# Performance work log

Hardware: AMD Instinct MI355X
Metric: run time of the kernel (lower is better)

The kernel has to match this reference:

```python
import jax, jax.numpy as jnp
import numpy as np
import math

B, S, D, H = 2, 2048, 1024, 16
DK = D // H


def setup_inputs() -> dict:
    key = jax.random.key(0)
    ks = jax.random.split(key, 11)
    f = jnp.float32
    return {
        "query": jax.random.normal(ks[0], (B, S, D), f),
        "key": jax.random.normal(ks[1], (B, S, D), f),
        "value": jax.random.normal(ks[2], (B, S, D), f),
        "wq": jax.random.normal(ks[3], (D, D), f) * 0.02,
        "bq": jnp.zeros((D,), f),
        "wk": jax.random.normal(ks[4], (D, D), f) * 0.02,
        "bk": jnp.zeros((D,), f),
        "wv": jax.random.normal(ks[5], (D, D), f) * 0.02,
        "bv": jnp.zeros((D,), f),
        "wo": jax.random.normal(ks[6], (D, D), f) * 0.02,
        "bo": jnp.zeros((D,), f),
    }


def reference(query, key, value, wq, bq, wk, bk, wv, bv, wo, bo):
    # Linear projections (torch Linear: y = x @ W.T + b)
    q = query @ wq.T + bq
    k = key @ wk.T + bk
    v = value @ wv.T + bv
    # [B,S,D] -> [B,H,S,DK]
    q = q.reshape(B, S, H, DK).transpose(0, 2, 1, 3)
    k = k.reshape(B, S, H, DK).transpose(0, 2, 1, 3)
    v = v.reshape(B, S, H, DK).transpose(0, 2, 1, 3)
    scores = jnp.einsum("bhqd,bhkd->bhqk", q, k) / math.sqrt(DK)
    causal = jnp.triu(jnp.ones((S, S), dtype=bool), k=1)  # strict upper triangle masked
    scores = jnp.where(causal, -jnp.inf, scores)
    attn = jax.nn.softmax(scores, axis=-1)  # dropout is identity in eval (p=0)
    x = jnp.einsum("bhqk,bhkd->bhqd", attn, v)
    x = x.transpose(0, 2, 1, 3).reshape(B, S, D)
    return x @ wo.T + bo
```

## Files before the change

### kernel.cpp

```cpp
#include <hip/hip_runtime.h>
#include <math.h>

#define BB 2
#define SS 2048
#define DD 1024
#define HH 16
#define DKK 64
#define MM (BB * SS)
#define KK DD
#define VSTR 2176

typedef __attribute__((ext_vector_type(8))) short short8;
typedef __attribute__((ext_vector_type(4))) float floatx4;

__device__ inline unsigned short f2bf(float x) {
    unsigned int u = __float_as_uint(x);
    u += 0x7fffu + ((u >> 16) & 1u);
    return (unsigned short)(u >> 16);
}

__device__ inline unsigned int pkbf(float a, float b) {
    return (__float_as_uint(b) & 0xffff0000u) | (__float_as_uint(a) >> 16);
}

__device__ inline void cast4f(const float* __restrict__ in, unsigned short* __restrict__ out, int i) {
    const float4 v = *(const float4*)(in + i);
    unsigned long long pk = (unsigned long long)f2bf(v.x)
                          | ((unsigned long long)f2bf(v.y) << 16)
                          | ((unsigned long long)f2bf(v.z) << 32)
                          | ((unsigned long long)f2bf(v.w) << 48);
    *(unsigned long long*)(out + i) = pk;
}

__global__ __launch_bounds__(256) void cast_all(const float* __restrict__ q, const float* __restrict__ k,
                                                const float* __restrict__ v,
                                                const float* __restrict__ wq, const float* __restrict__ wk,
                                                const float* __restrict__ wv, const float* __restrict__ wo,
                                                unsigned short* __restrict__ oq, unsigned short* __restrict__ ok,
                                                unsigned short* __restrict__ ov,
                                                unsigned short* __restrict__ owq, unsigned short* __restrict__ owk,
                                                unsigned short* __restrict__ owv, unsigned short* __restrict__ owo) {
    const int tid = blockIdx.x * 256 + threadIdx.x;
    #pragma unroll
    for (int it = 0; it < 8; ++it) {
        const int g = tid + it * 524288;
        const float* in;
        unsigned short* out;
        int idx;
        if (g < 3145728) {
            const int w = g >> 20;
            idx = g & 1048575;
            in  = (w == 0) ? q : (w == 1) ? k : v;
            out = (w == 0) ? oq : (w == 1) ? ok : ov;
        } else {
            const int gw = g - 3145728;
            const int w = gw >> 18;
            idx = gw & 262143;
            in  = (w == 0) ? wq : (w == 1) ? wk : (w == 2) ? wv : wo;
            out = (w == 0) ? owq : (w == 1) ? owk : (w == 2) ? owv : owo;
        }
        cast4f(in, out, idx * 4);
    }
}

#define GLDS(gp, lp) __builtin_amdgcn_global_load_lds( \
    (const __attribute__((address_space(1))) void*)(gp), \
    (__attribute__((address_space(3))) void*)(lp), 16, 0, 0)

#define SCHED0() __builtin_amdgcn_sched_barrier(0)
#define BAR()    __builtin_amdgcn_s_barrier()
#define WAITL0() asm volatile("s_waitcnt lgkmcnt(0)" ::: "memory")
#define WAITV(n) asm volatile("s_waitcnt vmcnt(" #n ")" ::: "memory")

__device__ __forceinline__ void gemm128_body(const unsigned short* __restrict__ A,
                                             const unsigned short* __restrict__ W,
                                             int m0, int n0,
                                             unsigned short* __restrict__ As,
                                             unsigned short* __restrict__ Bs,
                                             floatx4 (&acc)[4][4]) {
    const int t    = threadIdx.x;
    const int lane = t & 63;
    const int wave = t >> 6;
    const int col  = lane & 15;
    const int quad = lane >> 4;
    const int wm   = (wave >> 1) * 64;
    const int wn   = (wave & 1) * 64;

    const int r  = t >> 3;
    const int cs = t & 7;

    const int sA0 = (quad ^ (col & 7)) * 8;
    const int sA1 = ((quad + 4) ^ (col & 7)) * 8;

    auto stage = [&](int kt, int pb) {
        const int k0 = kt * 64;
        #pragma unroll
        for (int g = 0; g < 4; ++g) {
            const int row = g * 32 + r;
            const int ksw = (cs ^ (row & 7)) * 8;
            GLDS(A + (size_t)(m0 + row) * KK + k0 + ksw,
                 &As[pb * (128 * 64) + row * 64 + cs * 8]);
        }
        #pragma unroll
        for (int g = 0; g < 4; ++g) {
            const int row = g * 32 + r;
            const int ksw = (cs ^ (row & 7)) * 8;
            GLDS(W + (size_t)(n0 + row) * KK + k0 + ksw,
                 &Bs[pb * (128 * 64) + row * 64 + cs * 8]);
        }
    };

    stage(0, 0);
    WAITV(0); SCHED0(); BAR(); SCHED0();

    const int NK = KK / 64;
    for (int kt = 0; kt < NK; ++kt) {
        const int p = kt & 1;
        if (kt + 1 < NK) stage(kt + 1, p ^ 1);

        const unsigned short* Ab = &As[p * (128 * 64)];
        const unsigned short* Bb = &Bs[p * (128 * 64)];
        short8 a0[4], a1[4], b0[4], b1[4];
        #pragma unroll
        for (int i = 0; i < 4; ++i) {
            const unsigned short* ar = Ab + (wm + i * 16 + col) * 64;
            a0[i] = *(const short8*)(ar + sA0);
            a1[i] = *(const short8*)(ar + sA1);
        }
        #pragma unroll
        for (int j = 0; j < 4; ++j) {
            const unsigned short* br = Bb + (wn + j * 16 + col) * 64;
            b0[j] = *(const short8*)(br + sA0);
            b1[j] = *(const short8*)(br + sA1);
        }

        __builtin_amdgcn_s_setprio(1);
        #pragma unroll
        for (int i = 0; i < 4; ++i)
            #pragma unroll
            for (int j = 0; j < 4; ++j)
                acc[i][j] = __builtin_amdgcn_mfma_f32_16x16x32_bf16(a0[i], b0[j], acc[i][j], 0, 0, 0);
        #pragma unroll
        for (int i = 0; i < 4; ++i)
            #pragma unroll
            for (int j = 0; j < 4; ++j)
                acc[i][j] = __builtin_amdgcn_mfma_f32_16x16x32_bf16(a1[i], b1[j], acc[i][j], 0, 0, 0);
        __builtin_amdgcn_s_setprio(0);

        WAITL0(); SCHED0();
        if (kt + 1 < NK) { WAITV(0); }
        SCHED0(); BAR(); SCHED0();
    }
}

__global__ __launch_bounds__(256, 2) void gemm_qkv(const unsigned short* __restrict__ qB,
                                                   const unsigned short* __restrict__ kB,
                                                   const unsigned short* __restrict__ vB,
                                                   const unsigned short* __restrict__ wqB,
                                                   const unsigned short* __restrict__ wkB,
                                                   const unsigned short* __restrict__ wvB,
                                                   const float* __restrict__ bq,
                                                   const float* __restrict__ bk,
                                                   const float* __restrict__ bv,
                                                   unsigned short* __restrict__ Qh,
                                                   unsigned short* __restrict__ Kh,
                                                   unsigned short* __restrict__ Vt) {
    __shared__ __align__(16) unsigned short As[2 * 128 * 64];
    __shared__ __align__(16) unsigned short Bs[2 * 128 * 64];

    const int bid   = blockIdx.x;
    const int wgid  = (bid & 7) * 96 + (bid >> 3);
    const int which = wgid >> 8;
    const int tile  = wgid & 255;
    const int m0    = (tile >> 3) * 128;
    const int n0    = (tile & 7) * 128;

    const unsigned short* A = (which == 0) ? qB : (which == 1) ? kB : vB;
    const unsigned short* W = (which == 0) ? wqB : (which == 1) ? wkB : wvB;
    const float* bias       = (which == 0) ? bq : (which == 1) ? bk : bv;

    floatx4 acc[4][4] = {};
    gemm128_body(A, W, m0, n0, As, Bs, acc);

    const int t    = threadIdx.x;
    const int lane = t & 63;
    const int wave = t >> 6;
    const int col  = lane & 15;
    const int quad = lane >> 4;
    const int wm   = (wave >> 1) * 64;
    const int wn   = (wave & 1) * 64;

    #pragma unroll
    for (int i = 0; i < 4; ++i) {
        #pragma unroll
        for (int j = 0; j < 4; ++j) {
            const int n  = n0 + wn + j * 16 + col;
            const float bv0 = bias[n];
            const int h = n >> 6, dk = n & 63;
            const int mb  = m0 + wm + i * 16 + quad * 4;
            const int bdx = mb >> 11, s = mb & 2047;
            if (which != 2) {
                unsigned short* O = (which == 0) ? Qh : Kh;
                #pragma unroll
                for (int rr = 0; rr < 4; ++rr)
                    O[(((size_t)(bdx * HH + h)) * SS + (s + rr)) * DKK + dk] = f2bf(acc[i][j][rr] + bv0);
            } else {
                unsigned short* vp = Vt + (((size_t)(bdx * HH + h)) * DKK + dk) * VSTR + s;
                uint2 w;
                w.x = (unsigned int)f2bf(acc[i][j][0] + bv0) | ((unsigned int)f2bf(acc[i][j][1] + bv0) << 16);
                w.y = (unsigned int)f2bf(acc[i][j][2] + bv0) | ((unsigned int)f2bf(acc[i][j][3] + bv0) << 16);
                *(uint2*)vp = w;
            }
        }
    }
}

__global__ __launch_bounds__(256, 2) void gemm_out(const unsigned short* __restrict__ A,
                                                   const unsigned short* __restrict__ W,
                                                   const float* __restrict__ bias,
                                                   float* __restrict__ C) {
    __shared__ __align__(16) unsigned short As[2 * 128 * 64];
    __shared__ __align__(16) unsigned short Bs[2 * 128 * 64];

    const int bid  = blockIdx.x;
    const int wgid = (bid & 7) * 32 + (bid >> 3);
    const int m0   = (wgid >> 3) * 128;
    const int n0   = (wgid & 7) * 128;

    floatx4 acc[4][4] = {};
    gemm128_body(A, W, m0, n0, As, Bs, acc);

    const int t    = threadIdx.x;
    const int lane = t & 63;
    const int wave = t >> 6;
    const int col  = lane & 15;
    const int quad = lane >> 4;
    const int wm   = (wave >> 1) * 64;
    const int wn   = (wave & 1) * 64;

    #pragma unroll
    for (int i = 0; i < 4; ++i) {
        #pragma unroll
        for (int j = 0; j < 4; ++j) {
            const int n = n0 + wn + j * 16 + col;
            const float bv0 = bias[n];
            #pragma unroll
            for (int rr = 0; rr < 4; ++rr) {
                const int m = m0 + wm + i * 16 + quad * 4 + rr;
                C[(size_t)m * DD + n] = acc[i][j][rr] + bv0;
            }
        }
    }
}

#define C1 0.18033688011112042f
#define C2 11.541560327111707f
#define MFMA __builtin_amdgcn_mfma_f32_16x16x32_bf16

__global__ __launch_bounds__(512) void attn_mfma(const unsigned short* __restrict__ Qh,
                                                 const unsigned short* __restrict__ Kh,
                                                 const unsigned short* __restrict__ Vt,
                                                 unsigned short* __restrict__ X) {
    __shared__ __align__(16) unsigned short Ks[2][64 * 64];
    __shared__ __align__(16) unsigned short Vs[2][64 * 64];
    __shared__ __align__(16) unsigned short Plds[8][16 * 40];

    const int t    = threadIdx.x;
    const int lane = t & 63;
    const int wave = t >> 6;
    const int col  = lane & 15;
    const int quad = lane >> 4;

    const int lin = blockIdx.x;
    const int bh  = (lin & 7) + 8 * ((lin >> 3) & 3);
    const int pr  = lin >> 5;
    const int b   = bh / HH, h = bh % HH;

    const int cX  = (wave < 4) ? (31 - pr) : pr;
    const int q0  = cX * 64 + (wave & 3) * 16;
    const int nst = 32 - pr;

    const unsigned short* Kb = Kh + (size_t)bh * SS * DKK;
    const unsigned short* Vb = Vt + (size_t)bh * DKK * VSTR;

    const int r0  = t >> 3;
    const int sg0 = ((t & 7) ^ (r0 & 7)) * 8;

    unsigned short* Pw = &Plds[wave][0];

    const unsigned short* Qb = Qh + ((size_t)bh * SS + q0) * DKK;
    const short8 qa0 = *(const short8*)(Qb + (size_t)col * DKK + quad * 8);
    const short8 qa1 = *(const short8*)(Qb + (size_t)col * DKK + 32 + quad * 8);

    floatx4 o0 = {0.f, 0.f, 0.f, 0.f}, o1 = o0, o2 = o0, o3 = o0;
    float lp = 0.f;

    const int ksA = ((quad)      ^ (col & 7)) * 8;
    const int ksB = ((quad | 4)  ^ (col & 7)) * 8;

    GLDS(Kb + (size_t)r0 * DKK + sg0,  &Ks[0][t * 8]);
    GLDS(Vb + (size_t)r0 * VSTR + sg0, &Vs[0][t * 8]);

    int cur = 0;
    for (int kb = 0; kb < nst; ++kb) {
        __syncthreads();

        if (kb + 1 < nst) {
            const int jn = (kb + 1) * 64;
            const int nx = cur ^ 1;
            GLDS(Kb + (size_t)(jn + r0) * DKK + sg0,  &Ks[nx][t * 8]);
            GLDS(Vb + (size_t)r0 * VSTR + jn + sg0,   &Vs[nx][t * 8]);
        }

        const unsigned short* Kp = &Ks[cur][0];
        const unsigned short* Vp = &Vs[cur][0];

        #pragma unroll
        for (int hh = 0; hh < 2; ++hh) {
            const int j0 = kb * 64 + hh * 32;
            if (j0 < q0 + 16) {
                const short8 k0 = *(const short8*)(Kp + (hh * 32 + col) * 64 + ksA);
                const short8 k1 = *(const short8*)(Kp + (hh * 32 + col) * 64 + ksB);
                const short8 k2 = *(const short8*)(Kp + (hh * 32 + col + 16) * 64 + ksA);
                const short8 k3 = *(const short8*)(Kp + (hh * 32 + col + 16) * 64 + ksB);

                floatx4 t0 = {0.f, 0.f, 0.f, 0.f}, t1 = t0;
                __builtin_amdgcn_s_setprio(1);
                t0 = MFMA(k0, qa0, t0, 0, 0, 0);
                t0 = MFMA(k1, qa1, t0, 0, 0, 0);
                t1 = MFMA(k2, qa0, t1, 0, 0, 0);
                t1 = MFMA(k3, qa1, t1, 0, 0, 0);
                __builtin_amdgcn_s_setprio(0);

                float p[8];
                if (j0 + 31 > q0) {
                    const int lim = q0 + col - j0;
                    #pragma unroll
                    for (int r = 0; r < 4; ++r) {
                        p[r]     = (quad * 4 + r      <= lim) ? __builtin_exp2f(fmaf(t0[r], C1, -C2)) : 0.f;
                        p[4 + r] = (16 + quad * 4 + r <= lim) ? __builtin_exp2f(fmaf(t1[r], C1, -C2)) : 0.f;
                    }
                } else {
                    #pragma unroll
                    for (int r = 0; r < 4; ++r) {
                        p[r]     = __builtin_exp2f(fmaf(t0[r], C1, -C2));
                        p[4 + r] = __builtin_exp2f(fmaf(t1[r], C1, -C2));
                    }
                }
                lp += (p[0] + p[1]) + (p[2] + p[3]) + (p[4] + p[5]) + (p[6] + p[7]);

                uint2 w0 = { pkbf(p[0], p[1]), pkbf(p[2], p[3]) };
                uint2 w1 = { pkbf(p[4], p[5]), pkbf(p[6], p[7]) };
                *(uint2*)(Pw + col * 40 + quad * 4)      = w0;
                *(uint2*)(Pw + col * 40 + 16 + quad * 4) = w1;

                const short8 pb = *(const short8*)(Pw + col * 40 + quad * 8);
                const int vs = hh ? ksB : ksA;
                const short8 v0 = *(const short8*)(Vp + (col)      * 64 + vs);
                const short8 v1 = *(const short8*)(Vp + (col + 16) * 64 + vs);
                const short8 v2 = *(const short8*)(Vp + (col + 32) * 64 + vs);
                const short8 v3 = *(const short8*)(Vp + (col + 48) * 64 + vs);
                __builtin_amdgcn_s_setprio(1);
                o0 = MFMA(v0, pb, o0, 0, 0, 0);
                o1 = MFMA(v1, pb, o1, 0, 0, 0);
                o2 = MFMA(v2, pb, o2, 0, 0, 0);
                o3 = MFMA(v3, pb, o3, 0, 0, 0);
                __builtin_amdgcn_s_setprio(0);
            }
        }

        cur ^= 1;
    }

    lp += __shfl_xor(lp, 16, 64);
    lp += __shfl_xor(lp, 32, 64);
    const float li = 1.f / lp;

    unsigned short* Xp = X + ((size_t)(b * SS + q0 + col)) * DD + h * DKK + quad * 4;
    {
        uint2 w;
        w.x = (unsigned int)f2bf(o0[0] * li) | ((unsigned int)f2bf(o0[1] * li) << 16);
        w.y = (unsigned int)f2bf(o0[2] * li) | ((unsigned int)f2bf(o0[3] * li) << 16);
        *(uint2*)(Xp + 0) = w;
        w.x = (unsigned int)f2bf(o1[0] * li) | ((unsigned int)f2bf(o1[1] * li) << 16);
        w.y = (unsigned int)f2bf(o1[2] * li) | ((unsigned int)f2bf(o1[3] * li) << 16);
        *(uint2*)(Xp + 16) = w;
        w.x = (unsigned int)f2bf(o2[0] * li) | ((unsigned int)f2bf(o2[1] * li) << 16);
        w.y = (unsigned int)f2bf(o2[2] * li) | ((unsigned int)f2bf(o2[3] * li) << 16);
        *(uint2*)(Xp + 32) = w;
        w.x = (unsigned int)f2bf(o3[0] * li) | ((unsigned int)f2bf(o3[1] * li) << 16);
        w.y = (unsigned int)f2bf(o3[2] * li) | ((unsigned int)f2bf(o3[3] * li) << 16);
        *(uint2*)(Xp + 48) = w;
    }
}

extern "C" void kernel_launch(void* const* d_in, const int* in_sizes, int n_in,
                              void* d_out, int out_size, void* d_ws, size_t ws_size,
                              hipStream_t stream) {
    const float* query = (const float*)d_in[0];
    const float* key   = (const float*)d_in[1];
    const float* value = (const float*)d_in[2];
    const float* wq    = (const float*)d_in[3];
    const float* bq    = (const float*)d_in[4];
    const float* wk    = (const float*)d_in[5];
    const float* bk    = (const float*)d_in[6];
    const float* wv    = (const float*)d_in[7];
    const float* bv    = (const float*)d_in[8];
    const float* wo    = (const float*)d_in[9];
    const float* bo    = (const float*)d_in[10];

    char* ws = (char*)d_ws;
    const size_t MB = 1024 * 1024;
    unsigned short* qB  = (unsigned short*)(ws);
    unsigned short* kB  = (unsigned short*)(ws + 8 * MB);
    unsigned short* vB  = (unsigned short*)(ws + 16 * MB);
    unsigned short* wqB = (unsigned short*)(ws + 24 * MB);
    unsigned short* wkB = (unsigned short*)(ws + 26 * MB);
    unsigned short* wvB = (unsigned short*)(ws + 28 * MB);
    unsigned short* woB = (unsigned short*)(ws + 30 * MB);
    unsigned short* Qh  = (unsigned short*)(ws + 32 * MB);
    unsigned short* Kh  = (unsigned short*)(ws + 40 * MB);
    unsigned short* Vt  = (unsigned short*)(ws + 48 * MB);
    unsigned short* Xb  = qB;

    cast_all<<<2048, 256, 0, stream>>>(query, key, value, wq, wk, wv, wo,
                                       qB, kB, vB, wqB, wkB, wvB, woB);

    gemm_qkv<<<768, 256, 0, stream>>>(qB, kB, vB, wqB, wkB, wvB, bq, bk, bv, Qh, Kh, Vt);

    attn_mfma<<<512, 512, 0, stream>>>(Qh, Kh, Vt, Xb);

    gemm_out<<<256, 256, 0, stream>>>(Xb, woB, bo, (float*)d_out);
}
```

Measured before the change: 219.8 us.

## Restructure cast grid, vectorize Q/K epilogue via swapped MFMA, narrow out-GEMM tiles

The cast kernel now launches one block per 1024-element chunk instead of looping eight times per thread. The QKV GEMM swaps the MFMA operands for the Q/K path, so each lane holds four consecutive head dims and can write them as one packed 8-byte store instead of scalar 2-byte scatters. The output GEMM moves to 128x64 tiles with 512 blocks, which gives more waves on the device for a GEMM that only had 256 tiles. The cost is more launched blocks and lower per-block reuse of the A tile in the output GEMM.

```diff
diff --git a/kernel.cpp b/kernel.cpp
--- a/kernel.cpp
+++ b/kernel.cpp
@@ -23,6 +23,10 @@
     return (__float_as_uint(b) & 0xffff0000u) | (__float_as_uint(a) >> 16);
 }
 
+__device__ inline unsigned int pkbf_rne(float a, float b) {
+    return (unsigned int)f2bf(a) | ((unsigned int)f2bf(b) << 16);
+}
+
 __device__ inline void cast4f(const float* __restrict__ in, unsigned short* __restrict__ out, int i) {
     const float4 v = *(const float4*)(in + i);
     unsigned long long pk = (unsigned long long)f2bf(v.x)
@@ -40,27 +44,22 @@
                                                 unsigned short* __restrict__ ov,
                                                 unsigned short* __restrict__ owq, unsigned short* __restrict__ owk,
                                                 unsigned short* __restrict__ owv, unsigned short* __restrict__ owo) {
-    const int tid = blockIdx.x * 256 + threadIdx.x;
-    #pragma unroll
-    for (int it = 0; it < 8; ++it) {
-        const int g = tid + it * 524288;
-        const float* in;
-        unsigned short* out;
-        int idx;
-        if (g < 3145728) {
-            const int w = g >> 20;
-            idx = g & 1048575;
-            in  = (w == 0) ? q : (w == 1) ? k : v;
-            out = (w == 0) ? oq : (w == 1) ? ok : ov;
-        } else {
-            const int gw = g - 3145728;
-            const int w = gw >> 18;
-            idx = gw & 262143;
-            in  = (w == 0) ? wq : (w == 1) ? wk : (w == 2) ? wv : wo;
-            out = (w == 0) ? owq : (w == 1) ? owk : (w == 2) ? owv : owo;
-        }
-        cast4f(in, out, idx * 4);
-    }
+    const int blk = blockIdx.x;
+    const float* in;
+    unsigned short* out;
+    int idx;
+    if (blk < 12288) {
+        const int w = blk >> 12;
+        idx = blk & 4095;
+        in  = (w == 0) ? q : (w == 1) ? k : v;
+        out = (w == 0) ? oq : (w == 1) ? ok : ov;
+    } else {
+        const int w = (blk - 12288) >> 10;
+        idx = (blk - 12288) & 1023;
+        in  = (w == 0) ? wq : (w == 1) ? wk : (w == 2) ? wv : wo;
+        out = (w == 0) ? owq : (w == 1) ? owk : (w == 2) ? owv : owo;
+    }
+    cast4f(in, out, (idx * 256 + threadIdx.x) * 4);
 }
 
 #define GLDS(gp, lp) __builtin_amdgcn_global_load_lds( \
@@ -72,19 +71,21 @@
 #define WAITL0() asm volatile("s_waitcnt lgkmcnt(0)" ::: "memory")
 #define WAITV(n) asm volatile("s_waitcnt vmcnt(" #n ")" ::: "memory")
 
-__device__ __forceinline__ void gemm128_body(const unsigned short* __restrict__ A,
-                                             const unsigned short* __restrict__ W,
-                                             int m0, int n0,
-                                             unsigned short* __restrict__ As,
-                                             unsigned short* __restrict__ Bs,
-                                             floatx4 (&acc)[4][4]) {
+template<int BN, int SWAP>
+__device__ __forceinline__ void gemm_body2(const unsigned short* __restrict__ A,
+                                           const unsigned short* __restrict__ W,
+                                           int m0, int n0,
+                                           unsigned short* __restrict__ As,
+                                           unsigned short* __restrict__ Bs,
+                                           floatx4 (&acc)[4][BN / 32]) {
+    constexpr int NJ = BN / 32;
     const int t    = threadIdx.x;
     const int lane = t & 63;
     const int wave = t >> 6;
     const int col  = lane & 15;
     const int quad = lane >> 4;
     const int wm   = (wave >> 1) * 64;
-    const int wn   = (wave & 1) * 64;
+    const int wn   = (wave & 1) * (BN / 2);
 
     const int r  = t >> 3;
     const int cs = t & 7;
@@ -102,11 +103,11 @@
                  &As[pb * (128 * 64) + row * 64 + cs * 8]);
         }
         #pragma unroll
-        for (int g = 0; g < 4; ++g) {
+        for (int g = 0; g < BN / 32; ++g) {
             const int row = g * 32 + r;
             const int ksw = (cs ^ (row & 7)) * 8;
             GLDS(W + (size_t)(n0 + row) * KK + k0 + ksw,
-                 &Bs[pb * (128 * 64) + row * 64 + cs * 8]);
+                 &Bs[pb * (BN * 64) + row * 64 + cs * 8]);
         }
     };
 
@@ -119,8 +120,8 @@
         if (kt + 1 < NK) stage(kt + 1, p ^ 1);
 
         const unsigned short* Ab = &As[p * (128 * 64)];
-        const unsigned short* Bb = &Bs[p * (128 * 64)];
-        short8 a0[4], a1[4], b0[4], b1[4];
+        const unsigned short* Bb = &Bs[p * (BN * 64)];
+        short8 a0[4], a1[4], b0[NJ], b1[NJ];
         #pragma unroll
         for (int i = 0; i < 4; ++i) {
             const unsigned short* ar = Ab + (wm + i * 16 + col) * 64;
@@ -128,7 +129,7 @@
             a1[i] = *(const short8*)(ar + sA1);
         }
         #pragma unroll
-        for (int j = 0; j < 4; ++j) {
+        for (int j = 0; j < NJ; ++j) {
             const unsigned short* br = Bb + (wn + j * 16 + col) * 64;
             b0[j] = *(const short8*)(br + sA0);
             b1[j] = *(const short8*)(br + sA1);
@@ -138,13 +139,21 @@
         #pragma unroll
         for (int i = 0; i < 4; ++i)
             #pragma unroll
-            for (int j = 0; j < 4; ++j)
-                acc[i][j] = __builtin_amdgcn_mfma_f32_16x16x32_bf16(a0[i], b0[j], acc[i][j], 0, 0, 0);
+            for (int j = 0; j < NJ; ++j) {
+                if constexpr (SWAP)
+                    acc[i][j] = __builtin_amdgcn_mfma_f32_16x16x32_bf16(b0[j], a0[i], acc[i][j], 0, 0, 0);
+                else
+                    acc[i][j] = __builtin_amdgcn_mfma_f32_16x16x32_bf16(a0[i], b0[j], acc[i][j], 0, 0, 0);
+            }
         #pragma unroll
         for (int i = 0; i < 4; ++i)
             #pragma unroll
-            for (int j = 0; j < 4; ++j)
-                acc[i][j] = __builtin_amdgcn_mfma_f32_16x16x32_bf16(a1[i], b1[j], acc[i][j], 0, 0, 0);
+            for (int j = 0; j < NJ; ++j) {
+                if constexpr (SWAP)
+                    acc[i][j] = __builtin_amdgcn_mfma_f32_16x16x32_bf16(b1[j], a1[i], acc[i][j], 0, 0, 0);
+                else
+                    acc[i][j] = __builtin_amdgcn_mfma_f32_16x16x32_bf16(a1[i], b1[j], acc[i][j], 0, 0, 0);
+            }
         __builtin_amdgcn_s_setprio(0);
 
         WAITL0(); SCHED0();
@@ -179,9 +188,6 @@
     const unsigned short* W = (which == 0) ? wqB : (which == 1) ? wkB : wvB;
     const float* bias       = (which == 0) ? bq : (which == 1) ? bk : bv;
 
-    floatx4 acc[4][4] = {};
-    gemm128_body(A, W, m0, n0, As, Bs, acc);
-
     const int t    = threadIdx.x;
     const int lane = t & 63;
     const int wave = t >> 6;
@@ -190,25 +196,41 @@
     const int wm   = (wave >> 1) * 64;
     const int wn   = (wave & 1) * 64;
 
-    #pragma unroll
-    for (int i = 0; i < 4; ++i) {
-        #pragma unroll
-        for (int j = 0; j < 4; ++j) {
-            const int n  = n0 + wn + j * 16 + col;
-            const float bv0 = bias[n];
-            const int h = n >> 6, dk = n & 63;
-            const int mb  = m0 + wm + i * 16 + quad * 4;
+    floatx4 acc[4][4] = {};
+
+    if (which != 2) {
+        gemm_body2<128, 1>(A, W, m0, n0, As, Bs, acc);
+        unsigned short* O = (which == 0) ? Qh : Kh;
+        #pragma unroll
+        for (int i = 0; i < 4; ++i) {
+            const int mb  = m0 + wm + i * 16 + col;
             const int bdx = mb >> 11, s = mb & 2047;
-            if (which != 2) {
-                unsigned short* O = (which == 0) ? Qh : Kh;
-                #pragma unroll
-                for (int rr = 0; rr < 4; ++rr)
-                    O[(((size_t)(bdx * HH + h)) * SS + (s + rr)) * DKK + dk] = f2bf(acc[i][j][rr] + bv0);
-            } else {
+            #pragma unroll
+            for (int j = 0; j < 4; ++j) {
+                const int n  = n0 + wn + j * 16 + quad * 4;
+                const float4 b4 = *(const float4*)(bias + n);
+                const int h = n >> 6, dk = n & 63;
+                uint2 w;
+                w.x = pkbf_rne(acc[i][j][0] + b4.x, acc[i][j][1] + b4.y);
+                w.y = pkbf_rne(acc[i][j][2] + b4.z, acc[i][j][3] + b4.w);
+                *(uint2*)(O + (((size_t)(bdx * HH + h)) * SS + s) * DKK + dk) = w;
+            }
+        }
+    } else {
+        gemm_body2<128, 0>(A, W, m0, n0, As, Bs, acc);
+        #pragma unroll
+        for (int i = 0; i < 4; ++i) {
+            #pragma unroll
+            for (int j = 0; j < 4; ++j) {
+                const int n  = n0 + wn + j * 16 + col;
+                const float bv0 = bias[n];
+                const int h = n >> 6, dk = n & 63;
+                const int mb  = m0 + wm + i * 16 + quad * 4;
+                const int bdx = mb >> 11, s = mb & 2047;
                 unsigned short* vp = Vt + (((size_t)(bdx * HH + h)) * DKK + dk) * VSTR + s;
                 uint2 w;
-                w.x = (unsigned int)f2bf(acc[i][j][0] + bv0) | ((unsigned int)f2bf(acc[i][j][1] + bv0) << 16);
-                w.y = (unsigned int)f2bf(acc[i][j][2] + bv0) | ((unsigned int)f2bf(acc[i][j][3] + bv0) << 16);
+                w.x = pkbf_rne(acc[i][j][0] + bv0, acc[i][j][1] + bv0);
+                w.y = pkbf_rne(acc[i][j][2] + bv0, acc[i][j][3] + bv0);
                 *(uint2*)vp = w;
             }
         }
@@ -220,15 +242,15 @@
                                                    const float* __restrict__ bias,
                                                    float* __restrict__ C) {
     __shared__ __align__(16) unsigned short As[2 * 128 * 64];
-    __shared__ __align__(16) unsigned short Bs[2 * 128 * 64];
+    __shared__ __align__(16) unsigned short Bs[2 * 64 * 64];
 
     const int bid  = blockIdx.x;
-    const int wgid = (bid & 7) * 32 + (bid >> 3);
-    const int m0   = (wgid >> 3) * 128;
-    const int n0   = (wgid & 7) * 128;
-
-    floatx4 acc[4][4] = {};
-    gemm128_body(A, W, m0, n0, As, Bs, acc);
+    const int wgid = (bid & 7) * 64 + (bid >> 3);
+    const int m0   = (wgid >> 4) * 128;
+    const int n0   = (wgid & 15) * 64;
+
+    floatx4 acc[4][2] = {};
+    gemm_body2<64, 0>(A, W, m0, n0, As, Bs, acc);
 
     const int t    = threadIdx.x;
     const int lane = t & 63;
@@ -236,12 +258,12 @@
     const int col  = lane & 15;
     const int quad = lane >> 4;
     const int wm   = (wave >> 1) * 64;
-    const int wn   = (wave & 1) * 64;
+    const int wn   = (wave & 1) * 32;
 
     #pragma unroll
     for (int i = 0; i < 4; ++i) {
         #pragma unroll
-        for (int j = 0; j < 4; ++j) {
+        for (int j = 0; j < 2; ++j) {
             const int n = n0 + wn + j * 16 + col;
             const float bv0 = bias[n];
             #pragma unroll
@@ -336,15 +358,15 @@
                 if (j0 + 31 > q0) {
                     const int lim = q0 + col - j0;
                     #pragma unroll
-                    for (int r = 0; r < 4; ++r) {
-                        p[r]     = (quad * 4 + r      <= lim) ? __builtin_exp2f(fmaf(t0[r], C1, -C2)) : 0.f;
-                        p[4 + r] = (16 + quad * 4 + r <= lim) ? __builtin_exp2f(fmaf(t1[r], C1, -C2)) : 0.f;
+                    for (int rr = 0; rr < 4; ++rr) {
+                        p[rr]     = (quad * 4 + rr      <= lim) ? __builtin_exp2f(fmaf(t0[rr], C1, -C2)) : 0.f;
+                        p[4 + rr] = (16 + quad * 4 + rr <= lim) ? __builtin_exp2f(fmaf(t1[rr], C1, -C2)) : 0.f;
                     }
                 } else {
                     #pragma unroll
-                    for (int r = 0; r < 4; ++r) {
-                        p[r]     = __builtin_exp2f(fmaf(t0[r], C1, -C2));
-                        p[4 + r] = __builtin_exp2f(fmaf(t1[r], C1, -C2));
+                    for (int rr = 0; rr < 4; ++rr) {
+                        p[rr]     = __builtin_exp2f(fmaf(t0[rr], C1, -C2));
+                        p[4 + rr] = __builtin_exp2f(fmaf(t1[rr], C1, -C2));
                     }
                 }
                 lp += (p[0] + p[1]) + (p[2] + p[3]) + (p[4] + p[5]) + (p[6] + p[7]);
@@ -379,17 +401,17 @@
     unsigned short* Xp = X + ((size_t)(b * SS + q0 + col)) * DD + h * DKK + quad * 4;
     {
         uint2 w;
-        w.x = (unsigned int)f2bf(o0[0] * li) | ((unsigned int)f2bf(o0[1] * li) << 16);
-        w.y = (unsigned int)f2bf(o0[2] * li) | ((unsigned int)f2bf(o0[3] * li) << 16);
+        w.x = pkbf_rne(o0[0] * li, o0[1] * li);
+        w.y = pkbf_rne(o0[2] * li, o0[3] * li);
         *(uint2*)(Xp + 0) = w;
-        w.x = (unsigned int)f2bf(o1[0] * li) | ((unsigned int)f2bf(o1[1] * li) << 16);
-        w.y = (unsigned int)f2bf(o1[2] * li) | ((unsigned int)f2bf(o1[3] * li) << 16);
+        w.x = pkbf_rne(o1[0] * li, o1[1] * li);
+        w.y = pkbf_rne(o1[2] * li, o1[3] * li);
         *(uint2*)(Xp + 16) = w;
-        w.x = (unsigned int)f2bf(o2[0] * li) | ((unsigned int)f2bf(o2[1] * li) << 16);
-        w.y = (unsigned int)f2bf(o2[2] * li) | ((unsigned int)f2bf(o2[3] * li) << 16);
+        w.x = pkbf_rne(o2[0] * li, o2[1] * li);
+        w.y = pkbf_rne(o2[2] * li, o2[3] * li);
         *(uint2*)(Xp + 32) = w;
-        w.x = (unsigned int)f2bf(o3[0] * li) | ((unsigned int)f2bf(o3[1] * li) << 16);
-        w.y = (unsigned int)f2bf(o3[2] * li) | ((unsigned int)f2bf(o3[3] * li) << 16);
+        w.x = pkbf_rne(o3[0] * li, o3[1] * li);
+        w.y = pkbf_rne(o3[2] * li, o3[3] * li);
         *(uint2*)(Xp + 48) = w;
     }
 }
@@ -423,12 +445,12 @@
     unsigned short* Vt  = (unsigned short*)(ws + 48 * MB);
     unsigned short* Xb  = qB;
 
-    cast_all<<<2048, 256, 0, stream>>>(query, key, value, wq, wk, wv, wo,
-                                       qB, kB, vB, wqB, wkB, wvB, woB);
+    cast_all<<<16384, 256, 0, stream>>>(query, key, value, wq, wk, wv, wo,
+                                        qB, kB, vB, wqB, wkB, wvB, woB);
 
     gemm_qkv<<<768, 256, 0, stream>>>(qB, kB, vB, wqB, wkB, wvB, bq, bk, bv, Qh, Kh, Vt);
 
     attn_mfma<<<512, 512, 0, stream>>>(Qh, Kh, Vt, Xb);
 
-    gemm_out<<<256, 256, 0, stream>>>(Xb, woB, bo, (float*)d_out);
-}
+    gemm_out<<<512, 256, 0, stream>>>(Xb, woB, bo, (float*)d_out);
+}
```

Result: no change. 217.2 us (-1.2%).
